# Kernel optimization log

Hardware: AMD Instinct MI355X
Metric: run time of the kernel (lower is better)

## Reference

```python
import jax, jax.numpy as jnp
import numpy as np

M, K, N = 8192, 8192, 8192  # x:[M,K], weight:[N,K]
COMBINED_SCALE = 0.75  # scaling_factor(1.5) / 2 folded, as in the Triton kernel


def setup_inputs() -> dict:
    key = jax.random.key(0)
    kx, kw = jax.random.split(key)
    x = jax.random.normal(kx, (M, K), dtype=jnp.float32)
    weight = jax.random.normal(kw, (N, K), dtype=jnp.float32)
    return {"x": x, "weight": weight}


def reference(x, weight):
    # Algebraic identity: 1.5 * sum_j((x @ W^T)/2, axis=1, keepdims=True)
    #                   = 0.75 * x @ colsum(W)
    # Column-sum of weight over its N (hidden) rows -> [K]
    wcs = jnp.sum(weight, axis=0)  # fp32 accumulation
    # Per-row dot product -> [M, 1]
    y = COMBINED_SCALE * (x @ wcs)[:, None]
    return y
```

## Files before the change

kernel.cpp:

```cpp
#include <hip/hip_runtime.h>
#include <hip/hip_bf16.h>


#define M_DIM 8192
#define K_DIM 8192
#define N_DIM 8192

__global__ __launch_bounds__(256) void colsum_kernel(
    const float* __restrict__ w, float* __restrict__ wcs) {
    constexpr int ROWS = 64;
    const int col4 = blockIdx.x * 256 + threadIdx.x;
    const int row0 = blockIdx.y * ROWS;
    const int stride4 = K_DIM / 4;
    const float4* __restrict__ p =
        (const float4*)w + (size_t)row0 * stride4 + col4;

    float4 acc = make_float4(0.f, 0.f, 0.f, 0.f);
    #pragma unroll 8
    for (int r = 0; r < ROWS; ++r) {
        float4 v = p[(size_t)r * stride4];
        acc.x += v.x; acc.y += v.y; acc.z += v.z; acc.w += v.w;
    }
    float* out = wcs + col4 * 4;
    atomicAdd(out + 0, acc.x);
    atomicAdd(out + 1, acc.y);
    atomicAdd(out + 2, acc.z);
    atomicAdd(out + 3, acc.w);
}

__global__ __launch_bounds__(256) void rowdot_kernel(
    const float* __restrict__ x, const float* __restrict__ wcs,
    float* __restrict__ y) {
    const int m = blockIdx.x;
    const float4* __restrict__ x4 = (const float4*)(x + (size_t)m * K_DIM);
    const float4* __restrict__ w4 = (const float4*)wcs;

    float acc = 0.f;
    #pragma unroll 8
    for (int i = threadIdx.x; i < K_DIM / 4; i += 256) {
        float4 a = x4[i];
        float4 b = w4[i];
        acc += a.x * b.x + a.y * b.y + a.z * b.z + a.w * b.w;
    }
    #pragma unroll
    for (int off = 32; off > 0; off >>= 1)
        acc += __shfl_down(acc, off, 64);

    __shared__ float sacc[4];
    const int lane = threadIdx.x & 63;
    const int wave = threadIdx.x >> 6;
    if (lane == 0) sacc[wave] = acc;
    __syncthreads();
    if (threadIdx.x == 0) {
        y[m] = 0.75f * (sacc[0] + sacc[1] + sacc[2] + sacc[3]);
    }
}

extern "C" void kernel_launch(void* const* d_in, const int* in_sizes, int n_in,
                              void* d_out, int out_size, void* d_ws, size_t ws_size,
                              hipStream_t stream) {
    const float* x = (const float*)d_in[0];
    const float* w = (const float*)d_in[1];
    float* y = (float*)d_out;
    float* wcs = (float*)d_ws;

    hipMemsetAsync(wcs, 0, K_DIM * sizeof(float), stream);

    dim3 g1(K_DIM / 1024, N_DIM / 64);
    colsum_kernel<<<g1, 256, 0, stream>>>(w, wcs);

    rowdot_kernel<<<M_DIM, 256, 0, stream>>>(x, wcs, y);
}
```

Baseline: 504.0 us.

## Replace atomic column-sum accumulation with two-stage partial-sum reduction

The column sum of the weight matrix no longer uses float atomics into a memset buffer. Each block writes its per-chunk partial sums to a workspace, and a second kernel reduces the 128 partials per column. This drops the memset and the contended atomics, and makes the result deterministic. In exchange it adds a kernel launch and about 4 MB of extra workspace traffic, and the final reduce runs on only 8 blocks.

```diff
diff --git a/kernel.cpp b/kernel.cpp
--- a/kernel.cpp
+++ b/kernel.cpp
@@ -6,26 +6,38 @@
 #define K_DIM 8192
 #define N_DIM 8192
 
-__global__ __launch_bounds__(256) void colsum_kernel(
-    const float* __restrict__ w, float* __restrict__ wcs) {
-    constexpr int ROWS = 64;
+#define ROWCHUNKS 128
+#define ROWS_PER_CHUNK (N_DIM / ROWCHUNKS)
+#define K4 (K_DIM / 4)
+
+__global__ __launch_bounds__(256) void colsum_partial(
+    const float* __restrict__ w, float* __restrict__ partial) {
     const int col4 = blockIdx.x * 256 + threadIdx.x;
-    const int row0 = blockIdx.y * ROWS;
-    const int stride4 = K_DIM / 4;
+    const int row0 = blockIdx.y * ROWS_PER_CHUNK;
     const float4* __restrict__ p =
-        (const float4*)w + (size_t)row0 * stride4 + col4;
+        (const float4*)w + (size_t)row0 * K4 + col4;
 
     float4 acc = make_float4(0.f, 0.f, 0.f, 0.f);
     #pragma unroll 8
-    for (int r = 0; r < ROWS; ++r) {
-        float4 v = p[(size_t)r * stride4];
+    for (int r = 0; r < ROWS_PER_CHUNK; ++r) {
+        float4 v = p[(size_t)r * K4];
         acc.x += v.x; acc.y += v.y; acc.z += v.z; acc.w += v.w;
     }
-    float* out = wcs + col4 * 4;
-    atomicAdd(out + 0, acc.x);
-    atomicAdd(out + 1, acc.y);
-    atomicAdd(out + 2, acc.z);
-    atomicAdd(out + 3, acc.w);
+    ((float4*)partial)[(size_t)blockIdx.y * K4 + col4] = acc;
+}
+
+__global__ __launch_bounds__(256) void reduce_partials(
+    const float* __restrict__ partial, float* __restrict__ wcs) {
+    const int col4 = blockIdx.x * 256 + threadIdx.x;
+    const float4* __restrict__ p4 = (const float4*)partial;
+
+    float4 acc = make_float4(0.f, 0.f, 0.f, 0.f);
+    #pragma unroll 8
+    for (int c = 0; c < ROWCHUNKS; ++c) {
+        float4 v = p4[(size_t)c * K4 + col4];
+        acc.x += v.x; acc.y += v.y; acc.z += v.z; acc.w += v.w;
+    }
+    ((float4*)wcs)[col4] = acc;
 }
 
 __global__ __launch_bounds__(256) void rowdot_kernel(
@@ -37,7 +49,7 @@
 
     float acc = 0.f;
     #pragma unroll 8
-    for (int i = threadIdx.x; i < K_DIM / 4; i += 256) {
+    for (int i = threadIdx.x; i < K4; i += 256) {
         float4 a = x4[i];
         float4 b = w4[i];
         acc += a.x * b.x + a.y * b.y + a.z * b.z + a.w * b.w;
@@ -62,12 +74,14 @@
     const float* x = (const float*)d_in[0];
     const float* w = (const float*)d_in[1];
     float* y = (float*)d_out;
-    float* wcs = (float*)d_ws;
 
-    hipMemsetAsync(wcs, 0, K_DIM * sizeof(float), stream);
+    float* partial = (float*)d_ws;
+    float* wcs     = (float*)d_ws + (size_t)ROWCHUNKS * K_DIM;
 
-    dim3 g1(K_DIM / 1024, N_DIM / 64);
-    colsum_kernel<<<g1, 256, 0, stream>>>(w, wcs);
+    dim3 g1(K4 / 256, ROWCHUNKS);
+    colsum_partial<<<g1, 256, 0, stream>>>(w, partial);
+
+    reduce_partials<<<K4 / 256, 256, 0, stream>>>(partial, wcs);
 
     rowdot_kernel<<<M_DIM, 256, 0, stream>>>(x, wcs, y);
 }
```

New measurement: 510.0 us. No clear change (+1.2%).
